# Optimization experiments

Measured on AMD Instinct MI355X. Metric: run time of the kernel, lower is better.

The kernel has to match this reference:

```python
import jax, jax.numpy as jnp
import numpy as np

N_NODES = 50000
N_EDGES = 1600000
F_IN = 128
HIDDEN = 128
NUM_GRAPHS = 64


def _glorot(key, shape):
    fan_in = shape[0]
    return (jax.random.normal(key, shape, dtype=jnp.float32) / np.sqrt(fan_in)).astype(jnp.float32)


def setup_inputs() -> dict:
    key = jax.random.key(0)
    ks = jax.random.split(key, 16)
    x = jax.random.normal(ks[0], (N_NODES, F_IN), dtype=jnp.float32)
    edge_index = jax.random.randint(ks[1], (2, N_EDGES), 0, N_NODES, dtype=jnp.int64)
    batch = jnp.sort(jax.random.randint(ks[2], (N_NODES,), 0, NUM_GRAPHS, dtype=jnp.int64))
    # SAGEConv params: lin_l acts on aggregated neighbors, lin_r on root features.
    params = {
        'Wl0': _glorot(ks[3], (F_IN, HIDDEN)), 'Wr0': _glorot(ks[4], (F_IN, HIDDEN)), 'b0': jnp.zeros((HIDDEN,), jnp.float32),
        'Wl1': _glorot(ks[5], (HIDDEN, HIDDEN)), 'Wr1': _glorot(ks[6], (HIDDEN, HIDDEN)), 'b1': jnp.zeros((HIDDEN,), jnp.float32),
        'Wl2': _glorot(ks[7], (HIDDEN, HIDDEN)), 'Wr2': _glorot(ks[8], (HIDDEN, HIDDEN)), 'b2': jnp.zeros((HIDDEN,), jnp.float32),
        'W_lin1': _glorot(ks[9], (3 * HIDDEN, HIDDEN)), 'b_lin1': jnp.zeros((HIDDEN,), jnp.float32),
        'W_lin2': _glorot(ks[10], (HIDDEN, 2)), 'b_lin2': jnp.zeros((2,), jnp.float32),
    }
    return {'x': x, 'edge_index': edge_index, 'batch': batch, **params}


def _sage_conv(x, src, dst, Wl, Wr, b):
    # mean-aggregate neighbor (source) features at target nodes
    n = x.shape[0]
    deg = jax.ops.segment_sum(jnp.ones(src.shape, x.dtype), dst, num_segments=n)
    agg = jax.ops.segment_sum(x[src], dst, num_segments=n)
    agg = agg / jnp.maximum(deg, 1.0)[:, None]
    return agg @ Wl + x @ Wr + b


def reference(x, edge_index, batch,
              Wl0, Wr0, b0, Wl1, Wr1, b1, Wl2, Wr2, b2,
              W_lin1, b_lin1, W_lin2, b_lin2):
    src, dst = edge_index[0], edge_index[1]
    h = jax.nn.relu(_sage_conv(x, src, dst, Wl0, Wr0, b0))
    h = jax.nn.relu(_sage_conv(h, src, dst, Wl1, Wr1, b1))
    h = jax.nn.relu(_sage_conv(h, src, dst, Wl2, Wr2, b2))
    # global add / mean / max pool over graph ids
    add_p = jax.ops.segment_sum(h, batch, num_segments=NUM_GRAPHS)
    cnt = jax.ops.segment_sum(jnp.ones((h.shape[0],), h.dtype), batch, num_segments=NUM_GRAPHS)
    mean_p = add_p / jnp.maximum(cnt, 1.0)[:, None]
    max_p = jax.ops.segment_max(h, batch, num_segments=NUM_GRAPHS)
    g = jnp.concatenate([add_p, mean_p, max_p], axis=1)  # [G, 3*hidden]
    g = jax.nn.relu(g @ W_lin1 + b_lin1)
    # dropout p=0.5 is identity in eval mode
    logits = g @ W_lin2 + b_lin2
    return jax.nn.log_softmax(logits, axis=-1)
```

## Files before the change

kernel.cpp:

```cpp
#include <hip/hip_runtime.h>
#include <hip/hip_bf16.h>

#define N_NODES   50000
#define ZROW      N_NODES
#define F         128
#define NGRAPH    64
#define NB        391
#define B1        400
#define PADMAX    384

typedef __attribute__((ext_vector_type(8))) short    bf16x8;
typedef __attribute__((ext_vector_type(4))) float    f32x4;
typedef __attribute__((ext_vector_type(4))) unsigned u32x4;

__global__ __launch_bounds__(256) void bucket_hist(const int* __restrict__ dst,
                                                   int* __restrict__ bh, int nE, int chunk) {
    __shared__ int hist[NB];
    for (int i = threadIdx.x; i < NB; i += 256) hist[i] = 0;
    __syncthreads();
    int e0 = blockIdx.x * chunk;
    int e1 = min(e0 + chunk, nE);
    for (int e = e0 + threadIdx.x; e < e1; e += 256)
        atomicAdd(&hist[dst[e] >> 7], 1);
    __syncthreads();
    for (int i = threadIdx.x; i < NB; i += 256)
        bh[i * B1 + blockIdx.x] = hist[i];
}

__global__ __launch_bounds__(512) void scan_blocks(const int* __restrict__ bh,
                                                   int* __restrict__ boff,
                                                   int* __restrict__ btot) {
    __shared__ int s[512];
    int bkt = blockIdx.x, t = threadIdx.x;
    int v = (t < B1) ? bh[bkt * B1 + t] : 0;
    s[t] = v;
    __syncthreads();
    for (int off = 1; off < 512; off <<= 1) {
        int u = (t >= off) ? s[t - off] : 0;
        __syncthreads();
        s[t] += u;
        __syncthreads();
    }
    if (t < B1) boff[bkt * B1 + t] = s[t] - v;
    if (t == B1 - 1) btot[bkt] = s[t];
}

__global__ __launch_bounds__(512) void scan_buckets(const int* __restrict__ btot,
                                                    int* __restrict__ bbase) {
    __shared__ int s[512];
    int t = threadIdx.x;
    int v = (t < NB) ? btot[t] : 0;
    s[t] = v;
    __syncthreads();
    for (int off = 1; off < 512; off <<= 1) {
        int u = (t >= off) ? s[t - off] : 0;
        __syncthreads();
        s[t] += u;
        __syncthreads();
    }
    if (t < NB) bbase[t] = s[t] - v;
    if (t == NB - 1) bbase[NB] = s[t];
}

__global__ __launch_bounds__(256) void bucket_place(const int* __restrict__ src,
                                                    const int* __restrict__ dst,
                                                    const int* __restrict__ boff,
                                                    const int* __restrict__ bbase,
                                                    ushort2* __restrict__ ebuf, int nE, int chunk) {
    __shared__ int cur[NB];
    for (int i = threadIdx.x; i < NB; i += 256)
        cur[i] = bbase[i] + boff[i * B1 + blockIdx.x];
    __syncthreads();
    int e0 = blockIdx.x * chunk;
    int e1 = min(e0 + chunk, nE);
    for (int e = e0 + threadIdx.x; e < e1; e += 256) {
        int d = dst[e];
        int pos = atomicAdd(&cur[d >> 7], 1);
        ebuf[pos] = make_ushort2((unsigned short)src[e], (unsigned short)(d & 127));
    }
}

__global__ __launch_bounds__(256) void csr_build(const ushort2* __restrict__ ebuf,
                                                 const int* __restrict__ bbase,
                                                 int* __restrict__ row_ptr,
                                                 int* __restrict__ deg_arr,
                                                 unsigned short* __restrict__ csr, int n) {
    __shared__ int hist[128];
    __shared__ int cursor[128];
    __shared__ int pend[128];
    int b = blockIdx.x, t = threadIdx.x;
    int e0 = bbase[b], e1 = bbase[b + 1];
    if (t < 128) hist[t] = 0;
    __syncthreads();
    for (int e = e0 + t; e < e1; e += 256)
        atomicAdd(&hist[ebuf[e].y], 1);
    __syncthreads();
    if (t == 0) {
        int run = e0 + b * PADMAX;
        #pragma unroll 4
        for (int i = 0; i < 128; ++i) { cursor[i] = run; run += (hist[i] + 3) & ~3; }
    }
    __syncthreads();
    int node = b * 128 + t;
    if (t < 128) {
        pend[t] = cursor[t] + ((hist[t] + 3) & ~3);
        if (node < n) { row_ptr[node] = cursor[t]; deg_arr[node] = hist[t]; }
    }
    __syncthreads();
    for (int e = e0 + t; e < e1; e += 256) {
        ushort2 ed = ebuf[e];
        int pos = atomicAdd(&cursor[ed.y], 1);
        csr[pos] = ed.x;
    }
    __syncthreads();
    if (t < 128)
        for (int p = cursor[t]; p < pend[t]; ++p) csr[p] = (unsigned short)ZROW;
}

struct bh4 { __hip_bfloat16 a, b, c, d; };
__global__ __launch_bounds__(256) void cvt_kernel(const float* __restrict__ in,
                                                  __hip_bfloat16* __restrict__ out, long n4) {
    long i = (long)blockIdx.x * 256 + threadIdx.x;
    if (i >= n4) return;
    float4 v = ((const float4*)in)[i];
    bh4 o;
    o.a = __float2bfloat16(v.x);
    o.b = __float2bfloat16(v.y);
    o.c = __float2bfloat16(v.z);
    o.d = __float2bfloat16(v.w);
    ((bh4*)out)[i] = o;
}

__global__ __launch_bounds__(64) void zero_rows(__hip_bfloat16* __restrict__ xb,
                                                __hip_bfloat16* __restrict__ h1,
                                                __hip_bfloat16* __restrict__ h2) {
    int t = threadIdx.x;
    if (t < 48) {
        __hip_bfloat16* base = (t < 16) ? xb : (t < 32) ? h1 : h2;
        ((u32x4*)(base + (long)ZROW * F))[t & 15] = (u32x4){0, 0, 0, 0};
    }
}

__device__ __forceinline__ void acc8(float* a, u32x4 v) {
    a[0] += __uint_as_float(v.x << 16); a[1] += __uint_as_float(v.x & 0xffff0000u);
    a[2] += __uint_as_float(v.y << 16); a[3] += __uint_as_float(v.y & 0xffff0000u);
    a[4] += __uint_as_float(v.z << 16); a[5] += __uint_as_float(v.z & 0xffff0000u);
    a[6] += __uint_as_float(v.w << 16); a[7] += __uint_as_float(v.w & 0xffff0000u);
}

__global__ __launch_bounds__(256) void gather_kernel(const __hip_bfloat16* __restrict__ xin,
                                                     const int* __restrict__ row_ptr,
                                                     const int* __restrict__ deg_arr,
                                                     const unsigned short* __restrict__ csr,
                                                     __hip_bfloat16* __restrict__ agg, int n) {
    const int node = blockIdx.x * 4 + (threadIdx.x >> 6);
    if (node >= n) return;
    const int lane = threadIdx.x & 63;
    const int q = lane >> 4;
    const int r = lane & 15;

    const int beg = __builtin_nontemporal_load(&row_ptr[node]);
    const int d   = __builtin_nontemporal_load(&deg_arr[node]);
    const int end = beg + ((d + 3) & ~3);

    const u32x4* __restrict__ xr4 = (const u32x4*)xin;

    float a[8] = {}, b[8] = {};
    int i = beg;

    for (; i + 15 < end; i += 16) {
        int s0 = (int)__builtin_nontemporal_load(&csr[i + q]);
        int s1 = (int)__builtin_nontemporal_load(&csr[i + 4 + q]);
        int s2 = (int)__builtin_nontemporal_load(&csr[i + 8 + q]);
        int s3 = (int)__builtin_nontemporal_load(&csr[i + 12 + q]);
        u32x4 v0 = xr4[(unsigned)s0 * 16u + r];
        u32x4 v1 = xr4[(unsigned)s1 * 16u + r];
        u32x4 v2 = xr4[(unsigned)s2 * 16u + r];
        u32x4 v3 = xr4[(unsigned)s3 * 16u + r];
        acc8(a, v0);
        acc8(b, v1);
        acc8(a, v2);
        acc8(b, v3);
    }
    for (; i < end; i += 4) {
        int s0 = (int)__builtin_nontemporal_load(&csr[i + q]);
        u32x4 v0 = xr4[(unsigned)s0 * 16u + r];
        acc8(a, v0);
    }
    #pragma unroll
    for (int j = 0; j < 8; ++j) a[j] += b[j];

    #pragma unroll
    for (int j = 0; j < 8; ++j) {
        a[j] += __shfl_xor(a[j], 16);
        a[j] += __shfl_xor(a[j], 32);
    }

    if (q == 0) {
        float inv = 1.f / fmaxf((float)d, 1.f);
        u32x4 res;
        #pragma unroll
        for (int k = 0; k < 4; ++k) {
            __hip_bfloat16 lo = __float2bfloat16(a[2 * k]     * inv);
            __hip_bfloat16 hi = __float2bfloat16(a[2 * k + 1] * inv);
            res[k] = (unsigned)*(unsigned short*)&lo | ((unsigned)*(unsigned short*)&hi << 16);
        }
        __builtin_nontemporal_store(res, &((u32x4*)agg)[(long)node * 16 + r]);
    }
}

__global__ __launch_bounds__(256) void wfrag_all(const float* __restrict__ Wl0, const float* __restrict__ Wr0,
                                                 const float* __restrict__ Wl1, const float* __restrict__ Wr1,
                                                 const float* __restrict__ Wl2, const float* __restrict__ Wr2,
                                                 __hip_bfloat16* __restrict__ Wf) {
    int layer = blockIdx.x >> 4;
    int t = (blockIdx.x & 15) * 256 + threadIdx.x;
    const float* Wl = (layer == 0) ? Wl0 : (layer == 1) ? Wl1 : Wl2;
    const float* Wr = (layer == 0) ? Wr0 : (layer == 1) ? Wr1 : Wr2;
    int frag = t >> 6, lane = t & 63;
    int kstep = frag >> 3, ntg = frag & 7;
    int q = lane >> 4, r = lane & 15;
    bf16x8 v;
    #pragma unroll
    for (int j = 0; j < 8; ++j) {
        int krow = kstep * 32 + q * 8 + j;
        int col  = ntg * 16 + r;
        float f  = (krow < 128) ? Wl[krow * F + col] : Wr[(krow - 128) * F + col];
        __hip_bfloat16 h = __float2bfloat16(f);
        v[j] = *(short*)&h;
    }
    ((bf16x8*)(Wf + (long)layer * 32768))[t] = v;
}

__global__ __launch_bounds__(256) void sage_gemm(const __hip_bfloat16* __restrict__ aggb,
                                                 const __hip_bfloat16* __restrict__ hinb,
                                                 const __hip_bfloat16* __restrict__ Wf,
                                                 const float* __restrict__ bias,
                                                 __hip_bfloat16* __restrict__ hout, int n) {
    __shared__ bf16x8 sW[64 * 64];

    const int tid = threadIdx.x;
    #pragma unroll
    for (int it = 0; it < 16; ++it) {
        int idx = tid + it * 256;
        sW[idx] = ((const bf16x8*)Wf)[idx];
    }
    __syncthreads();

    const int w    = tid >> 6;
    const int lane = tid & 63;
    const int wr   = w >> 1, wc = w & 1;
    const int q    = lane >> 4, r = lane & 15;
    const int m0   = blockIdx.x * 64 + wr * 32;

    int rowA0 = m0 + r;        if (rowA0 >= n) rowA0 = 0;
    int rowA1 = m0 + 16 + r;   if (rowA1 >= n) rowA1 = 0;
    const long a0 = (long)rowA0 * 128 + q * 8;
    const long a1 = (long)rowA1 * 128 + q * 8;

    f32x4 acc[2][4];
    #pragma unroll
    for (int s = 0; s < 2; ++s)
        #pragma unroll
        for (int t = 0; t < 4; ++t) acc[s][t] = (f32x4){0.f, 0.f, 0.f, 0.f};

    #pragma unroll
    for (int kstep = 0; kstep < 8; ++kstep) {
        const __hip_bfloat16* base = (kstep < 4) ? aggb : hinb;
        const int ko = (kstep & 3) * 32;
        bf16x8 af0 = *(const bf16x8*)(base + a0 + ko);
        bf16x8 af1 = *(const bf16x8*)(base + a1 + ko);
        #pragma unroll
        for (int t = 0; t < 4; ++t) {
            bf16x8 bf = sW[(kstep * 8 + wc * 4 + t) * 64 + lane];
            acc[0][t] = __builtin_amdgcn_mfma_f32_16x16x32_bf16(af0, bf, acc[0][t], 0, 0, 0);
            acc[1][t] = __builtin_amdgcn_mfma_f32_16x16x32_bf16(af1, bf, acc[1][t], 0, 0, 0);
        }
    }

    #pragma unroll
    for (int t = 0; t < 4; ++t) {
        int col = wc * 64 + t * 16 + r;
        float bv = bias[col];
        #pragma unroll
        for (int s = 0; s < 2; ++s) {
            #pragma unroll
            for (int j = 0; j < 4; ++j) {
                int rowD = m0 + s * 16 + q * 4 + j;
                if (rowD < n) {
                    float v = fmaxf(acc[s][t][j] + bv, 0.f);
                    hout[(long)rowD * F + col] = __float2bfloat16(v);
                }
            }
        }
    }
}

__global__ __launch_bounds__(128) void pool_kernel(const __hip_bfloat16* __restrict__ h,
                                                   const int* __restrict__ batch,
                                                   float* __restrict__ add_p,
                                                   unsigned* __restrict__ max_p,
                                                   float* __restrict__ cnt, int n) {
    int start = blockIdx.x * 128;
    if (start >= n) return;
    int end = min(start + 128, n);
    int c = threadIdx.x;

    float s = 0.f, mx = 0.f, ct = 0.f;
    int g = batch[start];
    for (int m = start; m < end; ++m) {
        int gm = batch[m];
        if (gm != g) {
            atomicAdd(&add_p[g * F + c], s);
            atomicMax(&max_p[g * F + c], __float_as_uint(mx));
            if (c == 0) atomicAdd(&cnt[g], ct);
            s = 0.f; mx = 0.f; ct = 0.f; g = gm;
        }
        float v = __bfloat162float(h[(long)m * F + c]);
        s += v;
        mx = fmaxf(mx, v);
        ct += 1.f;
    }
    atomicAdd(&add_p[g * F + c], s);
    atomicMax(&max_p[g * F + c], __float_as_uint(mx));
    if (c == 0) atomicAdd(&cnt[g], ct);
}

__global__ __launch_bounds__(128) void head_kernel(const float* __restrict__ add_p,
                                                   const float* __restrict__ cnt,
                                                   const unsigned* __restrict__ max_p,
                                                   const float* __restrict__ W1,
                                                   const float* __restrict__ b1,
                                                   const float* __restrict__ W2,
                                                   const float* __restrict__ b2,
                                                   float* __restrict__ out) {
    int g = blockIdx.x, n = threadIdx.x;
    __shared__ float gv[384];
    float a    = add_p[g * F + n];
    float invc = 1.f / fmaxf(cnt[g], 1.f);
    gv[n]       = a;
    gv[128 + n] = a * invc;
    gv[256 + n] = __uint_as_float(max_p[g * F + n]);
    __syncthreads();

    float acc = b1[n];
    #pragma unroll 8
    for (int k = 0; k < 384; ++k) acc += gv[k] * W1[k * F + n];
    float r = fmaxf(acc, 0.f);

    float l0 = r * W2[n * 2 + 0];
    float l1 = r * W2[n * 2 + 1];
    #pragma unroll
    for (int off = 32; off > 0; off >>= 1) {
        l0 += __shfl_down(l0, off);
        l1 += __shfl_down(l1, off);
    }
    __shared__ float part[4];
    if ((n & 63) == 0) { part[(n >> 6) * 2] = l0; part[(n >> 6) * 2 + 1] = l1; }
    __syncthreads();
    if (n == 0) {
        float L0 = part[0] + part[2] + b2[0];
        float L1 = part[1] + part[3] + b2[1];
        float m  = fmaxf(L0, L1);
        float lse = m + logf(expf(L0 - m) + expf(L1 - m));
        out[g * 2 + 0] = L0 - lse;
        out[g * 2 + 1] = L1 - lse;
    }
}

extern "C" void kernel_launch(void* const* d_in, const int* in_sizes, int n_in,
                              void* d_out, int out_size, void* d_ws, size_t ws_size,
                              hipStream_t stream) {
    const float* x     = (const float*)d_in[0];
    const int*   ei    = (const int*)d_in[1];
    const int*   batch = (const int*)d_in[2];
    const float* Wl0 = (const float*)d_in[3];
    const float* Wr0 = (const float*)d_in[4];
    const float* b0  = (const float*)d_in[5];
    const float* Wl1 = (const float*)d_in[6];
    const float* Wr1 = (const float*)d_in[7];
    const float* b1  = (const float*)d_in[8];
    const float* Wl2 = (const float*)d_in[9];
    const float* Wr2 = (const float*)d_in[10];
    const float* b2  = (const float*)d_in[11];
    const float* W_lin1 = (const float*)d_in[12];
    const float* b_lin1 = (const float*)d_in[13];
    const float* W_lin2 = (const float*)d_in[14];
    const float* b_lin2 = (const float*)d_in[15];

    const int nE = in_sizes[1] / 2;
    const int* src = ei;
    const int* dst = ei + nE;

    const long TROWS = N_NODES + 16;
    char* p = (char*)d_ws;
    int*   row_ptr = (int*)p;            p += 50048 * 4;
    int*   deg_arr = (int*)p;            p += 50048 * 4;
    unsigned short* csr = (unsigned short*)p;  p += (((long)nE + (long)NB * PADMAX + 63) & ~63L) * 2;
    int*   bh      = (int*)p;            p += ((long)NB * B1 + 16) * 4;
    int*   boff    = (int*)p;            p += ((long)NB * B1 + 16) * 4;
    int*   btot    = (int*)p;            p += 512 * 4;
    int*   bbase   = (int*)p;            p += 512 * 4;
    __hip_bfloat16* xb   = (__hip_bfloat16*)p; p += TROWS * F * 2;
    __hip_bfloat16* aggb = (__hip_bfloat16*)p; p += TROWS * F * 2;
    __hip_bfloat16* h1b  = (__hip_bfloat16*)p; p += TROWS * F * 2;
    __hip_bfloat16* h2b  = (__hip_bfloat16*)p; p += TROWS * F * 2;
    __hip_bfloat16* h3b  = (__hip_bfloat16*)p; p += TROWS * F * 2;
    __hip_bfloat16* Wf   = (__hip_bfloat16*)p; p += 3L * 32768 * 2;
    float* add_p   = (float*)p;          p += NGRAPH * F * 4;
    unsigned* max_p = (unsigned*)p;      p += NGRAPH * F * 4;
    float* cnt     = (float*)p;          p += 256;

    ushort2* ebuf = (ushort2*)aggb;

    const int chunk = (nE + B1 - 1) / B1;
    const int gridG = (N_NODES + 63) / 64;
    const int gridW = (N_NODES + 3) / 4;
    const int gridP = (N_NODES + 127) / 128;
    const int gridC = (int)(((long)N_NODES * F / 4 + 255) / 256);

    bucket_hist <<<B1, 256, 0, stream>>>(dst, bh, nE, chunk);
    scan_blocks <<<NB, 512, 0, stream>>>(bh, boff, btot);
    scan_buckets<<<1,  512, 0, stream>>>(btot, bbase);
    bucket_place<<<B1, 256, 0, stream>>>(src, dst, boff, bbase, ebuf, nE, chunk);
    csr_build   <<<NB, 256, 0, stream>>>(ebuf, bbase, row_ptr, deg_arr, csr, N_NODES);

    cvt_kernel<<<gridC, 256, 0, stream>>>(x, xb, (long)N_NODES * F / 4);
    zero_rows<<<1, 64, 0, stream>>>(xb, h1b, h2b);
    wfrag_all<<<48, 256, 0, stream>>>(Wl0, Wr0, Wl1, Wr1, Wl2, Wr2, Wf);

    gather_kernel<<<gridW, 256, 0, stream>>>(xb, row_ptr, deg_arr, csr, aggb, N_NODES);
    sage_gemm<<<gridG, 256, 0, stream>>>(aggb, xb, Wf, b0, h1b, N_NODES);
    gather_kernel<<<gridW, 256, 0, stream>>>(h1b, row_ptr, deg_arr, csr, aggb, N_NODES);
    sage_gemm<<<gridG, 256, 0, stream>>>(aggb, h1b, Wf + 32768, b1, h2b, N_NODES);
    gather_kernel<<<gridW, 256, 0, stream>>>(h2b, row_ptr, deg_arr, csr, aggb, N_NODES);
    sage_gemm<<<gridG, 256, 0, stream>>>(aggb, h2b, Wf + 65536, b2, h3b, N_NODES);

    hipMemsetAsync(add_p, 0, (NGRAPH * F * 2 + NGRAPH) * sizeof(float), stream);
    pool_kernel<<<gridP, 128, 0, stream>>>(h3b, batch, add_p, max_p, cnt, N_NODES);

    head_kernel<<<NGRAPH, 128, 0, stream>>>(add_p, cnt, max_p,
                                            W_lin1, b_lin1, W_lin2, b_lin2,
                                            (float*)d_out);
}
```

Baseline: 320.3 us.

## Fuse neighbor gather, SAGE GEMM and graph pooling into one per-layer kernel

```diff
diff --git a/kernel.cpp b/kernel.cpp
--- a/kernel.cpp
+++ b/kernel.cpp
@@ -138,74 +138,6 @@
     if (t < 48) {
         __hip_bfloat16* base = (t < 16) ? xb : (t < 32) ? h1 : h2;
         ((u32x4*)(base + (long)ZROW * F))[t & 15] = (u32x4){0, 0, 0, 0};
-    }
-}
-
-__device__ __forceinline__ void acc8(float* a, u32x4 v) {
-    a[0] += __uint_as_float(v.x << 16); a[1] += __uint_as_float(v.x & 0xffff0000u);
-    a[2] += __uint_as_float(v.y << 16); a[3] += __uint_as_float(v.y & 0xffff0000u);
-    a[4] += __uint_as_float(v.z << 16); a[5] += __uint_as_float(v.z & 0xffff0000u);
-    a[6] += __uint_as_float(v.w << 16); a[7] += __uint_as_float(v.w & 0xffff0000u);
-}
-
-__global__ __launch_bounds__(256) void gather_kernel(const __hip_bfloat16* __restrict__ xin,
-                                                     const int* __restrict__ row_ptr,
-                                                     const int* __restrict__ deg_arr,
-                                                     const unsigned short* __restrict__ csr,
-                                                     __hip_bfloat16* __restrict__ agg, int n) {
-    const int node = blockIdx.x * 4 + (threadIdx.x >> 6);
-    if (node >= n) return;
-    const int lane = threadIdx.x & 63;
-    const int q = lane >> 4;
-    const int r = lane & 15;
-
-    const int beg = __builtin_nontemporal_load(&row_ptr[node]);
-    const int d   = __builtin_nontemporal_load(&deg_arr[node]);
-    const int end = beg + ((d + 3) & ~3);
-
-    const u32x4* __restrict__ xr4 = (const u32x4*)xin;
-
-    float a[8] = {}, b[8] = {};
-    int i = beg;
-
-    for (; i + 15 < end; i += 16) {
-        int s0 = (int)__builtin_nontemporal_load(&csr[i + q]);
-        int s1 = (int)__builtin_nontemporal_load(&csr[i + 4 + q]);
-        int s2 = (int)__builtin_nontemporal_load(&csr[i + 8 + q]);
-        int s3 = (int)__builtin_nontemporal_load(&csr[i + 12 + q]);
-        u32x4 v0 = xr4[(unsigned)s0 * 16u + r];
-        u32x4 v1 = xr4[(unsigned)s1 * 16u + r];
-        u32x4 v2 = xr4[(unsigned)s2 * 16u + r];
-        u32x4 v3 = xr4[(unsigned)s3 * 16u + r];
-        acc8(a, v0);
-        acc8(b, v1);
-        acc8(a, v2);
-        acc8(b, v3);
-    }
-    for (; i < end; i += 4) {
-        int s0 = (int)__builtin_nontemporal_load(&csr[i + q]);
-        u32x4 v0 = xr4[(unsigned)s0 * 16u + r];
-        acc8(a, v0);
-    }
-    #pragma unroll
-    for (int j = 0; j < 8; ++j) a[j] += b[j];
-
-    #pragma unroll
-    for (int j = 0; j < 8; ++j) {
-        a[j] += __shfl_xor(a[j], 16);
-        a[j] += __shfl_xor(a[j], 32);
-    }
-
-    if (q == 0) {
-        float inv = 1.f / fmaxf((float)d, 1.f);
-        u32x4 res;
-        #pragma unroll
-        for (int k = 0; k < 4; ++k) {
-            __hip_bfloat16 lo = __float2bfloat16(a[2 * k]     * inv);
-            __hip_bfloat16 hi = __float2bfloat16(a[2 * k + 1] * inv);
-            res[k] = (unsigned)*(unsigned short*)&lo | ((unsigned)*(unsigned short*)&hi << 16);
-        }
-        __builtin_nontemporal_store(res, &((u32x4*)agg)[(long)node * 16 + r]);
     }
 }
 
@@ -232,31 +164,87 @@
     ((bf16x8*)(Wf + (long)layer * 32768))[t] = v;
 }
 
-__global__ __launch_bounds__(256) void sage_gemm(const __hip_bfloat16* __restrict__ aggb,
-                                                 const __hip_bfloat16* __restrict__ hinb,
-                                                 const __hip_bfloat16* __restrict__ Wf,
-                                                 const float* __restrict__ bias,
-                                                 __hip_bfloat16* __restrict__ hout, int n) {
-    __shared__ bf16x8 sW[64 * 64];
-
-    const int tid = threadIdx.x;
-    #pragma unroll
+__device__ __forceinline__ void acc8(float* a, u32x4 v) {
+    a[0] += __uint_as_float(v.x << 16); a[1] += __uint_as_float(v.x & 0xffff0000u);
+    a[2] += __uint_as_float(v.y << 16); a[3] += __uint_as_float(v.y & 0xffff0000u);
+    a[4] += __uint_as_float(v.z << 16); a[5] += __uint_as_float(v.z & 0xffff0000u);
+    a[6] += __uint_as_float(v.w << 16); a[7] += __uint_as_float(v.w & 0xffff0000u);
+}
+
+__global__ __launch_bounds__(256) void sage_layer(const __hip_bfloat16* __restrict__ hin,
+                                                  const int* __restrict__ row_ptr,
+                                                  const int* __restrict__ deg_arr,
+                                                  const unsigned short* __restrict__ csr,
+                                                  const __hip_bfloat16* __restrict__ Wf,
+                                                  const float* __restrict__ bias,
+                                                  __hip_bfloat16* __restrict__ hout,
+                                                  const int* __restrict__ batch,
+                                                  float* __restrict__ add_p,
+                                                  unsigned* __restrict__ max_p,
+                                                  float* __restrict__ cnt,
+                                                  int n, int do_pool) {
+    __shared__ __align__(16) char sA[64 * 256];
+    __shared__ int sBatch[64];
+
+    const int tid  = threadIdx.x;
+    const int m0   = blockIdx.x * 64;
+    const int lane = tid & 63;
+    const int wv   = tid >> 6;
+    const int q    = lane >> 4, r = lane & 15;
+
+    const u32x4* __restrict__ xr4 = (const u32x4*)hin;
+
     for (int it = 0; it < 16; ++it) {
-        int idx = tid + it * 256;
-        sW[idx] = ((const bf16x8*)Wf)[idx];
-    }
-    __syncthreads();
-
-    const int w    = tid >> 6;
-    const int lane = tid & 63;
-    const int wr   = w >> 1, wc = w & 1;
-    const int q    = lane >> 4, r = lane & 15;
-    const int m0   = blockIdx.x * 64 + wr * 32;
-
-    int rowA0 = m0 + r;        if (rowA0 >= n) rowA0 = 0;
-    int rowA1 = m0 + 16 + r;   if (rowA1 >= n) rowA1 = 0;
-    const long a0 = (long)rowA0 * 128 + q * 8;
-    const long a1 = (long)rowA1 * 128 + q * 8;
+        const int nl   = wv * 16 + it;
+        const int node = m0 + nl;
+        float a[8] = {}, b[8] = {};
+        int d = 0;
+        if (node < n) {
+            const int beg = row_ptr[node];
+            d = deg_arr[node];
+            const int end = beg + ((d + 3) & ~3);
+            int i = beg;
+            for (; i + 7 < end; i += 8) {
+                int s0 = (int)__builtin_nontemporal_load(&csr[i + q]);
+                int s1 = (int)__builtin_nontemporal_load(&csr[i + 4 + q]);
+                u32x4 v0 = xr4[(unsigned)s0 * 16u + r];
+                u32x4 v1 = xr4[(unsigned)s1 * 16u + r];
+                acc8(a, v0);
+                acc8(b, v1);
+            }
+            for (; i < end; i += 4) {
+                int s0 = (int)__builtin_nontemporal_load(&csr[i + q]);
+                acc8(a, xr4[(unsigned)s0 * 16u + r]);
+            }
+        }
+        #pragma unroll
+        for (int j = 0; j < 8; ++j) a[j] += b[j];
+        #pragma unroll
+        for (int j = 0; j < 8; ++j) {
+            a[j] += __shfl_xor(a[j], 16);
+            a[j] += __shfl_xor(a[j], 32);
+        }
+        if (q == 0) {
+            float inv = 1.f / fmaxf((float)d, 1.f);
+            u32x4 res;
+            #pragma unroll
+            for (int k = 0; k < 4; ++k) {
+                __hip_bfloat16 lo = __float2bfloat16(a[2 * k]     * inv);
+                __hip_bfloat16 hi = __float2bfloat16(a[2 * k + 1] * inv);
+                res[k] = (unsigned)*(unsigned short*)&lo | ((unsigned)*(unsigned short*)&hi << 16);
+            }
+            *(u32x4*)(sA + nl * 256 + ((r ^ (nl & 7)) << 4)) = res;
+        }
+    }
+    if (do_pool && tid < 64 && m0 + tid < n) sBatch[tid] = batch[m0 + tid];
+    __syncthreads();
+
+    const int wr  = wv >> 1, wc = wv & 1;
+    const int rl0 = wr * 32 + r, rl1 = rl0 + 16;
+    int rowG0 = m0 + rl0; if (rowG0 >= n) rowG0 = 0;
+    int rowG1 = m0 + rl1; if (rowG1 >= n) rowG1 = 0;
+    const long gof0 = (long)rowG0 * 128 + q * 8;
+    const long gof1 = (long)rowG1 * 128 + q * 8;
 
     f32x4 acc[2][4];
     #pragma unroll
@@ -266,64 +254,84 @@
 
     #pragma unroll
     for (int kstep = 0; kstep < 8; ++kstep) {
-        const __hip_bfloat16* base = (kstep < 4) ? aggb : hinb;
-        const int ko = (kstep & 3) * 32;
-        bf16x8 af0 = *(const bf16x8*)(base + a0 + ko);
-        bf16x8 af1 = *(const bf16x8*)(base + a1 + ko);
+        bf16x8 af0, af1;
+        if (kstep < 4) {
+            af0 = *(const bf16x8*)(sA + rl0 * 256 + (((kstep * 4 + q) ^ (rl0 & 7)) << 4));
+            af1 = *(const bf16x8*)(sA + rl1 * 256 + (((kstep * 4 + q) ^ (rl1 & 7)) << 4));
+        } else {
+            const int ko = (kstep & 3) * 32;
+            af0 = *(const bf16x8*)(hin + gof0 + ko);
+            af1 = *(const bf16x8*)(hin + gof1 + ko);
+        }
         #pragma unroll
         for (int t = 0; t < 4; ++t) {
-            bf16x8 bf = sW[(kstep * 8 + wc * 4 + t) * 64 + lane];
+            bf16x8 bf = ((const bf16x8*)Wf)[(kstep * 8 + wc * 4 + t) * 64 + lane];
             acc[0][t] = __builtin_amdgcn_mfma_f32_16x16x32_bf16(af0, bf, acc[0][t], 0, 0, 0);
             acc[1][t] = __builtin_amdgcn_mfma_f32_16x16x32_bf16(af1, bf, acc[1][t], 0, 0, 0);
         }
     }
 
-    #pragma unroll
-    for (int t = 0; t < 4; ++t) {
-        int col = wc * 64 + t * 16 + r;
-        float bv = bias[col];
-        #pragma unroll
-        for (int s = 0; s < 2; ++s) {
+    if (!do_pool) {
+        #pragma unroll
+        for (int t = 0; t < 4; ++t) {
+            int col = wc * 64 + t * 16 + r;
+            float bv = bias[col];
             #pragma unroll
-            for (int j = 0; j < 4; ++j) {
-                int rowD = m0 + s * 16 + q * 4 + j;
-                if (rowD < n) {
+            for (int s = 0; s < 2; ++s) {
+                #pragma unroll
+                for (int j = 0; j < 4; ++j) {
+                    int rowD = m0 + s * 16 + q * 4 + j + wr * 32;
+                    if (rowD < n) {
+                        float v = fmaxf(acc[s][t][j] + bv, 0.f);
+                        hout[(long)rowD * F + col] = __float2bfloat16(v);
+                    }
+                }
+            }
+        }
+    } else {
+        __syncthreads();
+        __hip_bfloat16* sOut = (__hip_bfloat16*)sA;
+        #pragma unroll
+        for (int t = 0; t < 4; ++t) {
+            int col = wc * 64 + t * 16 + r;
+            float bv = bias[col];
+            #pragma unroll
+            for (int s = 0; s < 2; ++s) {
+                #pragma unroll
+                for (int j = 0; j < 4; ++j) {
+                    int rowl = wr * 32 + s * 16 + q * 4 + j;
                     float v = fmaxf(acc[s][t][j] + bv, 0.f);
-                    hout[(long)rowD * F + col] = __float2bfloat16(v);
+                    sOut[rowl * 128 + col] = __float2bfloat16(v);
                 }
             }
         }
-    }
-}
-
-__global__ __launch_bounds__(128) void pool_kernel(const __hip_bfloat16* __restrict__ h,
-                                                   const int* __restrict__ batch,
-                                                   float* __restrict__ add_p,
-                                                   unsigned* __restrict__ max_p,
-                                                   float* __restrict__ cnt, int n) {
-    int start = blockIdx.x * 128;
-    if (start >= n) return;
-    int end = min(start + 128, n);
-    int c = threadIdx.x;
-
-    float s = 0.f, mx = 0.f, ct = 0.f;
-    int g = batch[start];
-    for (int m = start; m < end; ++m) {
-        int gm = batch[m];
-        if (gm != g) {
-            atomicAdd(&add_p[g * F + c], s);
-            atomicMax(&max_p[g * F + c], __float_as_uint(mx));
-            if (c == 0) atomicAdd(&cnt[g], ct);
-            s = 0.f; mx = 0.f; ct = 0.f; g = gm;
-        }
-        float v = __bfloat162float(h[(long)m * F + c]);
-        s += v;
-        mx = fmaxf(mx, v);
-        ct += 1.f;
-    }
-    atomicAdd(&add_p[g * F + c], s);
-    atomicMax(&max_p[g * F + c], __float_as_uint(mx));
-    if (c == 0) atomicAdd(&cnt[g], ct);
+        __syncthreads();
+        const int colv = tid & 127, rh = tid >> 7;
+        float s = 0.f, mx = 0.f, ct = 0.f;
+        int g = -1;
+        for (int row = rh * 32; row < rh * 32 + 32; ++row) {
+            int m = m0 + row;
+            if (m >= n) break;
+            int gm = sBatch[row];
+            if (gm != g) {
+                if (g >= 0) {
+                    atomicAdd(&add_p[g * F + colv], s);
+                    atomicMax(&max_p[g * F + colv], __float_as_uint(mx));
+                    if (colv == 0) atomicAdd(&cnt[g], ct);
+                }
+                s = 0.f; mx = 0.f; ct = 0.f; g = gm;
+            }
+            float v = __bfloat162float(sOut[row * 128 + colv]);
+            s += v;
+            mx = fmaxf(mx, v);
+            ct += 1.f;
+        }
+        if (g >= 0) {
+            atomicAdd(&add_p[g * F + colv], s);
+            atomicMax(&max_p[g * F + colv], __float_as_uint(mx));
+            if (colv == 0) atomicAdd(&cnt[g], ct);
+        }
+    }
 }
 
 __global__ __launch_bounds__(128) void head_kernel(const float* __restrict__ add_p,
@@ -401,22 +409,17 @@
     int*   boff    = (int*)p;            p += ((long)NB * B1 + 16) * 4;
     int*   btot    = (int*)p;            p += 512 * 4;
     int*   bbase   = (int*)p;            p += 512 * 4;
+    ushort2* ebuf  = (ushort2*)p;        p += ((long)nE + 16) * 4;
     __hip_bfloat16* xb   = (__hip_bfloat16*)p; p += TROWS * F * 2;
-    __hip_bfloat16* aggb = (__hip_bfloat16*)p; p += TROWS * F * 2;
     __hip_bfloat16* h1b  = (__hip_bfloat16*)p; p += TROWS * F * 2;
     __hip_bfloat16* h2b  = (__hip_bfloat16*)p; p += TROWS * F * 2;
-    __hip_bfloat16* h3b  = (__hip_bfloat16*)p; p += TROWS * F * 2;
     __hip_bfloat16* Wf   = (__hip_bfloat16*)p; p += 3L * 32768 * 2;
     float* add_p   = (float*)p;          p += NGRAPH * F * 4;
     unsigned* max_p = (unsigned*)p;      p += NGRAPH * F * 4;
     float* cnt     = (float*)p;          p += 256;
 
-    ushort2* ebuf = (ushort2*)aggb;
-
     const int chunk = (nE + B1 - 1) / B1;
-    const int gridG = (N_NODES + 63) / 64;
-    const int gridW = (N_NODES + 3) / 4;
-    const int gridP = (N_NODES + 127) / 128;
+    const int gridL = (N_NODES + 63) / 64;
     const int gridC = (int)(((long)N_NODES * F / 4 + 255) / 256);
 
     bucket_hist <<<B1, 256, 0, stream>>>(dst, bh, nE, chunk);
@@ -428,16 +431,14 @@
     cvt_kernel<<<gridC, 256, 0, stream>>>(x, xb, (long)N_NODES * F / 4);
     zero_rows<<<1, 64, 0, stream>>>(xb, h1b, h2b);
     wfrag_all<<<48, 256, 0, stream>>>(Wl0, Wr0, Wl1, Wr1, Wl2, Wr2, Wf);
-
-    gather_kernel<<<gridW, 256, 0, stream>>>(xb, row_ptr, deg_arr, csr, aggb, N_NODES);
-    sage_gemm<<<gridG, 256, 0, stream>>>(aggb, xb, Wf, b0, h1b, N_NODES);
-    gather_kernel<<<gridW, 256, 0, stream>>>(h1b, row_ptr, deg_arr, csr, aggb, N_NODES);
-    sage_gemm<<<gridG, 256, 0, stream>>>(aggb, h1b, Wf + 32768, b1, h2b, N_NODES);
-    gather_kernel<<<gridW, 256, 0, stream>>>(h2b, row_ptr, deg_arr, csr, aggb, N_NODES);
-    sage_gemm<<<gridG, 256, 0, stream>>>(aggb, h2b, Wf + 65536, b2, h3b, N_NODES);
-
     hipMemsetAsync(add_p, 0, (NGRAPH * F * 2 + NGRAPH) * sizeof(float), stream);
-    pool_kernel<<<gridP, 128, 0, stream>>>(h3b, batch, add_p, max_p, cnt, N_NODES);
+
+    sage_layer<<<gridL, 256, 0, stream>>>(xb,  row_ptr, deg_arr, csr, Wf,         b0, h1b,
+                                          batch, add_p, max_p, cnt, N_NODES, 0);
+    sage_layer<<<gridL, 256, 0, stream>>>(h1b, row_ptr, deg_arr, csr, Wf + 32768, b1, h2b,
+                                          batch, add_p, max_p, cnt, N_NODES, 0);
+    sage_layer<<<gridL, 256, 0, stream>>>(h2b, row_ptr, deg_arr, csr, Wf + 65536, b2, (__hip_bfloat16*)nullptr,
+                                          batch, add_p, max_p, cnt, N_NODES, 1);
 
     head_kernel<<<NGRAPH, 128, 0, stream>>>(add_p, cnt, max_p,
                                             W_lin1, b_lin1, W_lin2, b_lin2,
```

Result: slower. 351.7 us (+9.8%).

## Fuse global pooling into last SAGE GEMM and read weights from global

Applied to the files above, without the earlier changes.

```diff
diff --git a/kernel.cpp b/kernel.cpp
--- a/kernel.cpp
+++ b/kernel.cpp
@@ -167,7 +167,6 @@
 
     float a[8] = {}, b[8] = {};
     int i = beg;
-
     for (; i + 15 < end; i += 16) {
         int s0 = (int)__builtin_nontemporal_load(&csr[i + q]);
         int s1 = (int)__builtin_nontemporal_load(&csr[i + 4 + q]);
@@ -236,22 +235,24 @@
                                                  const __hip_bfloat16* __restrict__ hinb,
                                                  const __hip_bfloat16* __restrict__ Wf,
                                                  const float* __restrict__ bias,
-                                                 __hip_bfloat16* __restrict__ hout, int n) {
-    __shared__ bf16x8 sW[64 * 64];
-
-    const int tid = threadIdx.x;
-    #pragma unroll
-    for (int it = 0; it < 16; ++it) {
-        int idx = tid + it * 256;
-        sW[idx] = ((const bf16x8*)Wf)[idx];
-    }
-    __syncthreads();
-
+                                                 __hip_bfloat16* __restrict__ hout,
+                                                 const int* __restrict__ batch,
+                                                 float* __restrict__ add_p,
+                                                 unsigned* __restrict__ max_p,
+                                                 float* __restrict__ cnt,
+                                                 int n, int do_pool) {
+    __shared__ __align__(16) __hip_bfloat16 sOut[64 * 128];
+    __shared__ int sBatch[64];
+
+    const int tid  = threadIdx.x;
+    const int base = blockIdx.x * 64;
     const int w    = tid >> 6;
     const int lane = tid & 63;
     const int wr   = w >> 1, wc = w & 1;
     const int q    = lane >> 4, r = lane & 15;
-    const int m0   = blockIdx.x * 64 + wr * 32;
+    const int m0   = base + wr * 32;
+
+    if (do_pool && tid < 64 && base + tid < n) sBatch[tid] = batch[base + tid];
 
     int rowA0 = m0 + r;        if (rowA0 >= n) rowA0 = 0;
     int rowA1 = m0 + 16 + r;   if (rowA1 >= n) rowA1 = 0;
@@ -264,66 +265,80 @@
         #pragma unroll
         for (int t = 0; t < 4; ++t) acc[s][t] = (f32x4){0.f, 0.f, 0.f, 0.f};
 
+    const bf16x8* __restrict__ Wv = (const bf16x8*)Wf;
     #pragma unroll
     for (int kstep = 0; kstep < 8; ++kstep) {
-        const __hip_bfloat16* base = (kstep < 4) ? aggb : hinb;
+        const __hip_bfloat16* basep = (kstep < 4) ? aggb : hinb;
         const int ko = (kstep & 3) * 32;
-        bf16x8 af0 = *(const bf16x8*)(base + a0 + ko);
-        bf16x8 af1 = *(const bf16x8*)(base + a1 + ko);
+        bf16x8 af0 = *(const bf16x8*)(basep + a0 + ko);
+        bf16x8 af1 = *(const bf16x8*)(basep + a1 + ko);
         #pragma unroll
         for (int t = 0; t < 4; ++t) {
-            bf16x8 bf = sW[(kstep * 8 + wc * 4 + t) * 64 + lane];
+            bf16x8 bf = Wv[(kstep * 8 + wc * 4 + t) * 64 + lane];
             acc[0][t] = __builtin_amdgcn_mfma_f32_16x16x32_bf16(af0, bf, acc[0][t], 0, 0, 0);
             acc[1][t] = __builtin_amdgcn_mfma_f32_16x16x32_bf16(af1, bf, acc[1][t], 0, 0, 0);
         }
     }
 
-    #pragma unroll
-    for (int t = 0; t < 4; ++t) {
-        int col = wc * 64 + t * 16 + r;
-        float bv = bias[col];
+    if (!do_pool) {
         #pragma unroll
-        for (int s = 0; s < 2; ++s) {
+        for (int t = 0; t < 4; ++t) {
+            int col = wc * 64 + t * 16 + r;
+            float bv = bias[col];
             #pragma unroll
-            for (int j = 0; j < 4; ++j) {
-                int rowD = m0 + s * 16 + q * 4 + j;
-                if (rowD < n) {
-                    float v = fmaxf(acc[s][t][j] + bv, 0.f);
-                    hout[(long)rowD * F + col] = __float2bfloat16(v);
+            for (int s = 0; s < 2; ++s) {
+                #pragma unroll
+                for (int j = 0; j < 4; ++j) {
+                    int rowD = m0 + s * 16 + q * 4 + j;
+                    if (rowD < n) {
+                        float v = fmaxf(acc[s][t][j] + bv, 0.f);
+                        hout[(long)rowD * F + col] = __float2bfloat16(v);
+                    }
                 }
             }
         }
-    }
-}
-
-__global__ __launch_bounds__(128) void pool_kernel(const __hip_bfloat16* __restrict__ h,
-                                                   const int* __restrict__ batch,
-                                                   float* __restrict__ add_p,
-                                                   unsigned* __restrict__ max_p,
-                                                   float* __restrict__ cnt, int n) {
-    int start = blockIdx.x * 128;
-    if (start >= n) return;
-    int end = min(start + 128, n);
-    int c = threadIdx.x;
-
-    float s = 0.f, mx = 0.f, ct = 0.f;
-    int g = batch[start];
-    for (int m = start; m < end; ++m) {
-        int gm = batch[m];
-        if (gm != g) {
-            atomicAdd(&add_p[g * F + c], s);
-            atomicMax(&max_p[g * F + c], __float_as_uint(mx));
-            if (c == 0) atomicAdd(&cnt[g], ct);
-            s = 0.f; mx = 0.f; ct = 0.f; g = gm;
-        }
-        float v = __bfloat162float(h[(long)m * F + c]);
-        s += v;
-        mx = fmaxf(mx, v);
-        ct += 1.f;
-    }
-    atomicAdd(&add_p[g * F + c], s);
-    atomicMax(&max_p[g * F + c], __float_as_uint(mx));
-    if (c == 0) atomicAdd(&cnt[g], ct);
+    } else {
+        #pragma unroll
+        for (int t = 0; t < 4; ++t) {
+            int col = wc * 64 + t * 16 + r;
+            float bv = bias[col];
+            #pragma unroll
+            for (int s = 0; s < 2; ++s) {
+                #pragma unroll
+                for (int j = 0; j < 4; ++j) {
+                    int rowl = wr * 32 + s * 16 + q * 4 + j;
+                    float v = fmaxf(acc[s][t][j] + bv, 0.f);
+                    sOut[rowl * 128 + col] = __float2bfloat16(v);
+                }
+            }
+        }
+        __syncthreads();
+        const int colv = tid & 127, rh = tid >> 7;
+        float s = 0.f, mx = 0.f, ct = 0.f;
+        int g = -1;
+        for (int row = rh * 32; row < rh * 32 + 32; ++row) {
+            int m = base + row;
+            if (m >= n) break;
+            int gm = sBatch[row];
+            if (gm != g) {
+                if (g >= 0) {
+                    atomicAdd(&add_p[g * F + colv], s);
+                    atomicMax(&max_p[g * F + colv], __float_as_uint(mx));
+                    if (colv == 0) atomicAdd(&cnt[g], ct);
+                }
+                s = 0.f; mx = 0.f; ct = 0.f; g = gm;
+            }
+            float v = __bfloat162float(sOut[row * 128 + colv]);
+            s += v;
+            mx = fmaxf(mx, v);
+            ct += 1.f;
+        }
+        if (g >= 0) {
+            atomicAdd(&add_p[g * F + colv], s);
+            atomicMax(&max_p[g * F + colv], __float_as_uint(mx));
+            if (colv == 0) atomicAdd(&cnt[g], ct);
+        }
+    }
 }
 
 __global__ __launch_bounds__(128) void head_kernel(const float* __restrict__ add_p,
@@ -401,22 +416,19 @@
     int*   boff    = (int*)p;            p += ((long)NB * B1 + 16) * 4;
     int*   btot    = (int*)p;            p += 512 * 4;
     int*   bbase   = (int*)p;            p += 512 * 4;
+    ushort2* ebuf  = (ushort2*)p;        p += ((long)nE + 16) * 4;
     __hip_bfloat16* xb   = (__hip_bfloat16*)p; p += TROWS * F * 2;
     __hip_bfloat16* aggb = (__hip_bfloat16*)p; p += TROWS * F * 2;
     __hip_bfloat16* h1b  = (__hip_bfloat16*)p; p += TROWS * F * 2;
     __hip_bfloat16* h2b  = (__hip_bfloat16*)p; p += TROWS * F * 2;
-    __hip_bfloat16* h3b  = (__hip_bfloat16*)p; p += TROWS * F * 2;
     __hip_bfloat16* Wf   = (__hip_bfloat16*)p; p += 3L * 32768 * 2;
     float* add_p   = (float*)p;          p += NGRAPH * F * 4;
     unsigned* max_p = (unsigned*)p;      p += NGRAPH * F * 4;
     float* cnt     = (float*)p;          p += 256;
 
-    ushort2* ebuf = (ushort2*)aggb;
-
     const int chunk = (nE + B1 - 1) / B1;
     const int gridG = (N_NODES + 63) / 64;
     const int gridW = (N_NODES + 3) / 4;
-    const int gridP = (N_NODES + 127) / 128;
     const int gridC = (int)(((long)N_NODES * F / 4 + 255) / 256);
 
     bucket_hist <<<B1, 256, 0, stream>>>(dst, bh, nE, chunk);
@@ -428,16 +440,17 @@
     cvt_kernel<<<gridC, 256, 0, stream>>>(x, xb, (long)N_NODES * F / 4);
     zero_rows<<<1, 64, 0, stream>>>(xb, h1b, h2b);
     wfrag_all<<<48, 256, 0, stream>>>(Wl0, Wr0, Wl1, Wr1, Wl2, Wr2, Wf);
+    hipMemsetAsync(add_p, 0, (NGRAPH * F * 2 + NGRAPH) * sizeof(float), stream);
 
     gather_kernel<<<gridW, 256, 0, stream>>>(xb, row_ptr, deg_arr, csr, aggb, N_NODES);
-    sage_gemm<<<gridG, 256, 0, stream>>>(aggb, xb, Wf, b0, h1b, N_NODES);
+    sage_gemm<<<gridG, 256, 0, stream>>>(aggb, xb, Wf, b0, h1b,
+                                         batch, add_p, max_p, cnt, N_NODES, 0);
     gather_kernel<<<gridW, 256, 0, stream>>>(h1b, row_ptr, deg_arr, csr, aggb, N_NODES);
-    sage_gemm<<<gridG, 256, 0, stream>>>(aggb, h1b, Wf + 32768, b1, h2b, N_NODES);
+    sage_gemm<<<gridG, 256, 0, stream>>>(aggb, h1b, Wf + 32768, b1, h2b,
+                                         batch, add_p, max_p, cnt, N_NODES, 0);
     gather_kernel<<<gridW, 256, 0, stream>>>(h2b, row_ptr, deg_arr, csr, aggb, N_NODES);
-    sage_gemm<<<gridG, 256, 0, stream>>>(aggb, h2b, Wf + 65536, b2, h3b, N_NODES);
-
-    hipMemsetAsync(add_p, 0, (NGRAPH * F * 2 + NGRAPH) * sizeof(float), stream);
-    pool_kernel<<<gridP, 128, 0, stream>>>(h3b, batch, add_p, max_p, cnt, N_NODES);
+    sage_gemm<<<gridG, 256, 0, stream>>>(aggb, h2b, Wf + 65536, b2, (__hip_bfloat16*)nullptr,
+                                         batch, add_p, max_p, cnt, N_NODES, 1);
 
     head_kernel<<<NGRAPH, 128, 0, stream>>>(add_p, cnt, max_p,
                                             W_lin1, b_lin1, W_lin2, b_lin2,
```

After: 322.7 us. No clear change (+0.7%).
